# Optimization experiments

Measured on AMD Instinct MI355X. Metric: run time of the kernel, lower is better.

Reference implementation:

```python
import jax, jax.numpy as jnp
import numpy as np

D_MODEL = 1024
D_STATE = 16
D_CONV = 4
EXPAND = 2
HEADDIM = 8
D_INNER = EXPAND * D_MODEL            # 2048
NHEADS = D_INNER // HEADDIM           # 256
CONV_DIM = D_INNER + 2 * D_STATE      # 2080 (ngroups=1)
D_IN_PROJ = 2 * D_INNER + 2 * D_STATE + NHEADS  # 4384
B_SZ, SEQ = 4, 2048
EPS = 1e-5


def setup_inputs() -> dict:
    key = jax.random.key(0)
    ks = jax.random.split(key, 8)
    return {
        "x": jax.random.normal(ks[0], (B_SZ, SEQ, D_MODEL), jnp.float32),
        "ln_w": jnp.ones((D_MODEL,), jnp.float32),
        "ln_b": jnp.zeros((D_MODEL,), jnp.float32),
        "W_in": jax.random.normal(ks[1], (D_MODEL, D_IN_PROJ), jnp.float32) * 0.02,
        "conv_w": jax.random.normal(ks[2], (D_CONV, 1, CONV_DIM), jnp.float32) * 0.2,
        "conv_b": jnp.zeros((CONV_DIM,), jnp.float32),
        "A_log": jnp.log(jax.random.uniform(ks[3], (NHEADS,), jnp.float32, 1.0, 16.0)),
        "Dp": jnp.ones((NHEADS,), jnp.float32) + 0.1 * jax.random.normal(ks[4], (NHEADS,), jnp.float32),
        "dt_bias": 0.5 * jax.random.normal(ks[5], (NHEADS,), jnp.float32),
        "rms_w": jnp.ones((D_INNER,), jnp.float32),
        "W_out": jax.random.normal(ks[6], (D_INNER, D_MODEL), jnp.float32) * 0.02,
    }


def _mamba_block(x, ln_w, ln_b, W_in, conv_w, conv_b, A_log, Dp, dt_bias, rms_w, W_out):
    B, L, _ = x.shape
    # pre-norm LayerNorm
    mu = jnp.mean(x, axis=-1, keepdims=True)
    var = jnp.mean((x - mu) ** 2, axis=-1, keepdims=True)
    xn = (x - mu) * jax.lax.rsqrt(var + EPS) * ln_w + ln_b

    # in_proj -> z, xBC, dt
    u = xn @ W_in                                    # (B, L, 4384)
    z = u[..., :D_INNER]
    xBC = u[..., D_INNER:D_INNER + CONV_DIM]
    dt = jax.nn.softplus(u[..., -NHEADS:] + dt_bias)  # (B, L, NHEADS)

    # causal depthwise conv1d + SiLU
    xp = jnp.pad(xBC, ((0, 0), (D_CONV - 1, 0), (0, 0)))
    xBC = jax.lax.conv_general_dilated(
        xp, conv_w, window_strides=(1,), padding="VALID",
        dimension_numbers=("NWC", "WIO", "NWC"), feature_group_count=CONV_DIM)
    xBC = jax.nn.silu(xBC + conv_b)

    xs = xBC[..., :D_INNER].reshape(B, L, NHEADS, HEADDIM)   # SSM input
    Bm = xBC[..., D_INNER:D_INNER + D_STATE]                  # (B, L, N)
    Cm = xBC[..., D_INNER + D_STATE:]                          # (B, L, N)

    A = -jnp.exp(A_log)                                       # (NHEADS,)

    def step(h, inp):
        # h: (B, H, P, N)
        x_t, B_t, C_t, dt_t = inp
        dA = jnp.exp(dt_t * A)                                 # (B, H)
        h = h * dA[..., None, None] + jnp.einsum("bh,bhp,bn->bhpn", dt_t, x_t, B_t)
        y = jnp.einsum("bhpn,bn->bhp", h, C_t)
        return h, y

    h0 = jnp.zeros((B, NHEADS, HEADDIM, D_STATE), x.dtype)
    _, ys = jax.lax.scan(step, h0, (xs.swapaxes(0, 1), Bm.swapaxes(0, 1),
                                     Cm.swapaxes(0, 1), dt.swapaxes(0, 1)))
    y = ys.swapaxes(0, 1) + Dp[None, None, :, None] * xs       # (B, L, H, P)
    y = y.reshape(B, L, D_INNER)

    # gated RMSNorm: rmsnorm(y * silu(z)) * weight
    g = y * jax.nn.silu(z)
    g = g * jax.lax.rsqrt(jnp.mean(g * g, axis=-1, keepdims=True) + EPS) * rms_w

    return x + g @ W_out


def reference(x, ln_w, ln_b, W_in, conv_w, conv_b, A_log, Dp, dt_bias, rms_w, W_out):
    return _mamba_block(x, ln_w, ln_b, W_in, conv_w, conv_b, A_log, Dp, dt_bias, rms_w, W_out)
```

## Files before the change

kernel.cpp:

```cpp
#include <hip/hip_runtime.h>

typedef __bf16 bf16;
typedef __attribute__((ext_vector_type(8))) __bf16 bf16x8;
typedef __attribute__((ext_vector_type(4))) float f32x4;

#define B_SZ 4
#define SEQ 2048
#define DM 1024
#define DIN 2048
#define NH 256
#define DSTATE 16
#define CONVD 2080
#define DPROJ 4384
#define NPAD1 4608
#define MROWS 8192
#define NC 64
#define LC 32
#define UROWB 8768

__device__ __forceinline__ void gload_lds16(const void* g, void* l) {
  __builtin_amdgcn_global_load_lds(
      (__attribute__((address_space(1))) void*)g,
      (__attribute__((address_space(3))) void*)l, 16, 0, 0);
}

template <int N>
__device__ __forceinline__ void vm_wait() {
  asm volatile("s_waitcnt vmcnt(%0)" ::"n"(N) : "memory");
}
__device__ __forceinline__ void bar() { asm volatile("s_barrier" ::: "memory"); }
__device__ __forceinline__ void lgkm0() {
  asm volatile("s_waitcnt lgkmcnt(0)" ::: "memory");
}

__global__ void transpose_cvt(const float* __restrict__ W, bf16* __restrict__ WT,
                              int K, int N, int Npad) {
  __shared__ float tile[32][33];
  int k0 = blockIdx.x * 32, n0 = blockIdx.y * 32;
  int tx = threadIdx.x, ty = threadIdx.y;
#pragma unroll
  for (int j = 0; j < 4; j++) {
    int k = k0 + ty + 8 * j, n = n0 + tx;
    tile[ty + 8 * j][tx] = (k < K && n < N) ? W[(size_t)k * N + n] : 0.f;
  }
  __syncthreads();
#pragma unroll
  for (int j = 0; j < 4; j++) {
    int n = n0 + ty + 8 * j, k = k0 + tx;
    if (n < Npad && k < K) WT[(size_t)n * K + k] = (bf16)tile[tx][ty + 8 * j];
  }
}

__global__ __launch_bounds__(256) void ln_kernel(const float* __restrict__ x,
                                                 const float* __restrict__ lw,
                                                 const float* __restrict__ lb,
                                                 bf16* __restrict__ xn) {
  int row = blockIdx.x;
  int t = threadIdx.x;
  f32x4 v4 = ((const f32x4*)(x + (size_t)row * DM))[t];
  float v0 = v4[0], v1 = v4[1], v2 = v4[2], v3 = v4[3];
  float s = v0 + v1 + v2 + v3;
  float s2 = v0 * v0 + v1 * v1 + v2 * v2 + v3 * v3;
#pragma unroll
  for (int off = 32; off > 0; off >>= 1) {
    s += __shfl_down(s, off);
    s2 += __shfl_down(s2, off);
  }
  __shared__ float ps[8];
  int wave = t >> 6, lane = t & 63;
  if (lane == 0) { ps[wave] = s; ps[4 + wave] = s2; }
  __syncthreads();
  s = ps[0] + ps[1] + ps[2] + ps[3];
  s2 = ps[4] + ps[5] + ps[6] + ps[7];
  float mean = s * (1.f / DM);
  float var = s2 * (1.f / DM) - mean * mean;
  float rstd = rsqrtf(var + 1e-5f);
  f32x4 wv = ((const f32x4*)lw)[t];
  f32x4 bv = ((const f32x4*)lb)[t];
  bf16 o[4];
  o[0] = (bf16)((v0 - mean) * rstd * wv[0] + bv[0]);
  o[1] = (bf16)((v1 - mean) * rstd * wv[1] + bv[1]);
  o[2] = (bf16)((v2 - mean) * rstd * wv[2] + bv[2]);
  o[3] = (bf16)((v3 - mean) * rstd * wv[3] + bv[3]);
  bf16* dst = xn + (size_t)row * DM + t * 4;
  dst[0] = o[0]; dst[1] = o[1]; dst[2] = o[2]; dst[3] = o[3];
}

__global__ __launch_bounds__(512, 2) void gemm1_8p(const bf16* __restrict__ A,
                                                   const bf16* __restrict__ BT,
                                                   bf16* __restrict__ C) {
  __shared__ char lds[139264];
  int bid = blockIdx.x;
  int xcd = bid & 7;
  int l = bid >> 3;
  int bm = xcd * 4 + ((l >> 3) & 3);
  int bn = (l >> 5) * 8 + (l & 7);
  int m0 = bm * 256, n0 = bn * 192;
  int t = threadIdx.x, lane = t & 63, wave = t >> 6;
  int wm = wave >> 2, wn = wave & 3;
  int lr16 = lane & 15, kq = lane >> 4;
  int ts0 = kq ^ (lr16 & 7);
  int ts1 = (4 + kq) ^ (lr16 & 7);
  int sw = (lane & 7) ^ (lane >> 3);
  int l8 = lane >> 3;
  const char* Ab = (const char*)A;
  const char* Bb = (const char*)BT;

  auto stA = [&](int kt) {
    char* slot = lds + (kt & 1) * 32768;
    size_t ko = (size_t)kt * 128 + sw * 16;
#pragma unroll
    for (int g = 0; g < 4; g++) {
      int c = wave * 4 + g;
      gload_lds16(Ab + (size_t)(m0 + c * 8 + l8) * 2048 + ko, slot + c * 1024);
    }
  };
  auto stB = [&](int kt) {
    char* slot = lds + 65536 + (kt % 3) * 24576;
    size_t ko = (size_t)kt * 128 + sw * 16;
#pragma unroll
    for (int g = 0; g < 3; g++) {
      int c = wave * 3 + g;
      gload_lds16(Bb + (size_t)(n0 + c * 8 + l8) * 2048 + ko, slot + c * 1024);
    }
  };

  f32x4 acc[8][3] = {};
  bf16x8 a_[4][2], b_[3][2];

  stA(0); stB(0); stA(1); stB(1);
  vm_wait<7>();
  bar();
#pragma unroll 1
  for (int kt = 0; kt < 16; kt++) {
    {
      const char* sa = lds + (kt & 1) * 32768;
      const char* sb = lds + 65536 + (kt % 3) * 24576;
#pragma unroll
      for (int mi = 0; mi < 4; mi++) {
        int lrow = wm * 128 + mi * 16 + lr16;
        a_[mi][0] = *(const bf16x8*)(sa + lrow * 128 + ts0 * 16);
        a_[mi][1] = *(const bf16x8*)(sa + lrow * 128 + ts1 * 16);
      }
#pragma unroll
      for (int ni = 0; ni < 3; ni++) {
        int lrow = wn * 48 + ni * 16 + lr16;
        b_[ni][0] = *(const bf16x8*)(sb + lrow * 128 + ts0 * 16);
        b_[ni][1] = *(const bf16x8*)(sb + lrow * 128 + ts1 * 16);
      }
      if (kt >= 1 && kt < 15) stA(kt + 1);
      if (kt < 14) stB(kt + 2);
      bar();
      lgkm0();
      __builtin_amdgcn_s_setprio(1);
#pragma unroll
      for (int mi = 0; mi < 4; mi++)
#pragma unroll
        for (int ni = 0; ni < 3; ni++) {
          acc[mi][ni] = __builtin_amdgcn_mfma_f32_16x16x32_bf16(a_[mi][0], b_[ni][0], acc[mi][ni], 0, 0, 0);
          acc[mi][ni] = __builtin_amdgcn_mfma_f32_16x16x32_bf16(a_[mi][1], b_[ni][1], acc[mi][ni], 0, 0, 0);
        }
      __builtin_amdgcn_s_setprio(0);
      bar();
    }
    {
      const char* sa = lds + (kt & 1) * 32768;
#pragma unroll
      for (int mi = 0; mi < 4; mi++) {
        int lrow = wm * 128 + 64 + mi * 16 + lr16;
        a_[mi][0] = *(const bf16x8*)(sa + lrow * 128 + ts0 * 16);
        a_[mi][1] = *(const bf16x8*)(sa + lrow * 128 + ts1 * 16);
      }
      if (kt <= 13) vm_wait<3>();
      else if (kt == 14) vm_wait<0>();
      bar();
      lgkm0();
      __builtin_amdgcn_s_setprio(1);
#pragma unroll
      for (int mi = 0; mi < 4; mi++)
#pragma unroll
        for (int ni = 0; ni < 3; ni++) {
          acc[4 + mi][ni] = __builtin_amdgcn_mfma_f32_16x16x32_bf16(a_[mi][0], b_[ni][0], acc[4 + mi][ni], 0, 0, 0);
          acc[4 + mi][ni] = __builtin_amdgcn_mfma_f32_16x16x32_bf16(a_[mi][1], b_[ni][1], acc[4 + mi][ni], 0, 0, 0);
        }
      __builtin_amdgcn_s_setprio(0);
      bar();
    }
  }
#pragma unroll
  for (int fr = 0; fr < 8; fr++)
#pragma unroll
    for (int ni = 0; ni < 3; ni++) {
      int row = m0 + wm * 128 + fr * 16 + kq * 4;
      int col = n0 + wn * 48 + ni * 16 + lr16;
      f32x4 v = acc[fr][ni];
      if (col < 4384) {
#pragma unroll
        for (int r = 0; r < 4; r++)
          C[(size_t)(row + r) * DPROJ + col] = (bf16)v[r];
      }
    }
}

#define G2_PHASE(MQ, P, STAGE, VMW)                                                        \
  {                                                                                        \
    const char* sa_ = lds + ((P) * 2 + (MQ)) * 16384;                                      \
    const char* sb_ = lds + 65536 + (P) * 16384;                                           \
    bf16x8 a_[4][2], b_[2][2];                                                             \
    _Pragma("unroll") for (int mi = 0; mi < 4; mi++) {                                     \
      int lrow = wm * 64 + mi * 16 + lr16;                                                 \
      a_[mi][0] = *(const bf16x8*)(sa_ + lrow * 128 + ts0 * 16);                           \
      a_[mi][1] = *(const bf16x8*)(sa_ + lrow * 128 + ts1 * 16);                           \
    }                                                                                      \
    _Pragma("unroll") for (int ni = 0; ni < 2; ni++) {                                     \
      int lrow = wn * 32 + ni * 16 + lr16;                                                 \
      b_[ni][0] = *(const bf16x8*)(sb_ + lrow * 128 + ts0 * 16);                           \
      b_[ni][1] = *(const bf16x8*)(sb_ + lrow * 128 + ts1 * 16);                           \
    }                                                                                      \
    STAGE;                                                                                 \
    VMW;                                                                                   \
    bar();                                                                                 \
    lgkm0();                                                                               \
    __builtin_amdgcn_s_setprio(1);                                                         \
    _Pragma("unroll") for (int mi = 0; mi < 4; mi++)                                       \
      _Pragma("unroll") for (int ni = 0; ni < 2; ni++) {                                   \
        acc[(MQ) * 4 + mi][ni] = __builtin_amdgcn_mfma_f32_16x16x32_bf16(                  \
            a_[mi][0], b_[ni][0], acc[(MQ) * 4 + mi][ni], 0, 0, 0);                        \
        acc[(MQ) * 4 + mi][ni] = __builtin_amdgcn_mfma_f32_16x16x32_bf16(                  \
            a_[mi][1], b_[ni][1], acc[(MQ) * 4 + mi][ni], 0, 0, 0);                        \
      }                                                                                    \
    __builtin_amdgcn_s_setprio(0);                                                         \
    bar();                                                                                 \
  }

__global__ __launch_bounds__(512, 2) void gemm2_8p(const bf16* __restrict__ A,
                                                   const bf16* __restrict__ BT,
                                                   float* __restrict__ C,
                                                   const float* __restrict__ Xres) {
  __shared__ char lds[98304];
  int bid = blockIdx.x;
  int swz = (bid & 7) * 32 + (bid >> 3);
  int bm = swz >> 3, bn = swz & 7;
  int m0 = bm * 256, n0 = bn * 128;
  int t = threadIdx.x, lane = t & 63, wave = t >> 6;
  int wm = wave >> 2, wn = wave & 3;
  int lr16 = lane & 15, kq = lane >> 4;
  int ts0 = kq ^ (lr16 & 7);
  int ts1 = (4 + kq) ^ (lr16 & 7);
  int sw = (lane & 7) ^ ((lane >> 3) & 7);
  int l8 = lane >> 3;
  int c0 = 2 * wave, c1 = 2 * wave + 1;
  int lr0 = c0 * 8 + l8, lr1 = c1 * 8 + l8;
  const char* Ab = (const char*)A;
  const char* Bb = (const char*)BT;
  int grA0 = m0 + (lr0 >> 6) * 128 + (lr0 & 63);
  int grA1 = m0 + (lr1 >> 6) * 128 + (lr1 & 63);
  int gcB0 = n0 + lr0, gcB1 = n0 + lr1;

  auto stA = [&](int kt, int p, int mq) {
    char* slot = lds + (p * 2 + mq) * 16384;
    size_t ko = (size_t)kt * 128 + sw * 16;
    gload_lds16(Ab + (size_t)(grA0 + mq * 64) * 4096 + ko, slot + c0 * 1024);
    gload_lds16(Ab + (size_t)(grA1 + mq * 64) * 4096 + ko, slot + c1 * 1024);
  };
  auto stB = [&](int kt, int p) {
    char* slot = lds + 65536 + p * 16384;
    size_t ko = (size_t)kt * 128 + sw * 16;
    gload_lds16(Bb + (size_t)gcB0 * 4096 + ko, slot + c0 * 1024);
    gload_lds16(Bb + (size_t)gcB1 * 4096 + ko, slot + c1 * 1024);
  };

  f32x4 acc[8][2] = {};
  stA(0, 0, 0); stB(0, 0); stA(0, 0, 1); stA(1, 1, 0);
  vm_wait<4>();
  bar();
#pragma unroll 1
  for (int kt = 0; kt < 32; kt++) {
    int p = kt & 1;
    G2_PHASE(0, p, { if (kt + 1 < 32) { stB(kt + 1, p ^ 1); stA(kt + 1, p ^ 1, 1); } },
             { if (kt < 31) vm_wait<6>(); else vm_wait<0>(); });
    G2_PHASE(1, p, { if (kt + 2 < 32) stA(kt + 2, p, 0); },
             { if (kt < 30) vm_wait<4>(); else if (kt == 30) vm_wait<2>(); });
  }
#pragma unroll
  for (int mq = 0; mq < 2; mq++)
#pragma unroll
    for (int mi = 0; mi < 4; mi++)
#pragma unroll
      for (int ni = 0; ni < 2; ni++) {
        int row = m0 + wm * 128 + mq * 64 + mi * 16 + kq * 4;
        int col = n0 + wn * 32 + ni * 16 + lr16;
        f32x4 v = acc[mq * 4 + mi][ni];
#pragma unroll
        for (int r = 0; r < 4; r++) {
          size_t o = (size_t)(row + r) * DM + col;
          C[o] = Xres[o] + v[r];
        }
      }
}

__global__ __launch_bounds__(256) void conv_prep3(const bf16* __restrict__ u,
                                                  const float* __restrict__ cw,
                                                  const float* __restrict__ cb,
                                                  const float* __restrict__ dt_bias,
                                                  bf16* __restrict__ xs,
                                                  float* __restrict__ BC,
                                                  float* __restrict__ dtf) {
  const int JPR = 292;
  int idx = blockIdx.x * 256 + threadIdx.x;
  if (idx >= MROWS * JPR) return;
  int row = idx / JPR;
  int j = idx - row * JPR;
  int t = row & (SEQ - 1);
  if (j < 260) {
    int c0 = j * 8;
    float acc[8];
#pragma unroll
    for (int i = 0; i < 8; i++) acc[i] = cb[c0 + i];
    const bf16* ub = u + (size_t)row * DPROJ + DIN + c0;
#pragma unroll
    for (int tap = 0; tap < 4; tap++) {
      int tt = t - 3 + tap;
      if (tt >= 0) {
        bf16x8 uv = *(const bf16x8*)(ub + (ptrdiff_t)(tap - 3) * DPROJ);
        const float* wv = cw + tap * CONVD + c0;
#pragma unroll
        for (int i = 0; i < 8; i++) acc[i] += wv[i] * (float)uv[i];
      }
    }
    if (c0 < DIN) {
      bf16x8 o;
#pragma unroll
      for (int i = 0; i < 8; i++) {
        float sv = acc[i] / (1.f + __expf(-acc[i]));
        o[i] = (bf16)sv;
      }
      *(bf16x8*)(xs + (size_t)row * DIN + c0) = o;
    } else {
      float* bc = BC + (size_t)row * 32 + (c0 - DIN);
#pragma unroll
      for (int i = 0; i < 8; i++) bc[i] = acc[i] / (1.f + __expf(-acc[i]));
    }
  } else {
    int h0 = (j - 260) * 8;
    bf16x8 uv = *(const bf16x8*)(u + (size_t)row * DPROJ + (DPROJ - NH) + h0);
    float* dst = dtf + (size_t)row * NH + h0;
#pragma unroll
    for (int i = 0; i < 8; i++) {
      float xv = (float)uv[i] + dt_bias[h0 + i];
      dst[i] = (xv > 20.f) ? xv : log1pf(__expf(xv));
    }
  }
}

__global__ __launch_bounds__(64) void scan_p1(const bf16* __restrict__ xs,
                                              const float* __restrict__ BC,
                                              const float* __restrict__ dtf,
                                              const float* __restrict__ A_log,
                                              bf16* __restrict__ uscr) {
  int c = blockIdx.x & 63, hg = (blockIdx.x >> 6) & 31, b = blockIdx.x >> 11;
  int lane = threadIdx.x, hh = lane >> 3;
  int h = hg * 8 + hh;
  float A = -__expf(A_log[h]);
  float st[16];
#pragma unroll
  for (int n = 0; n < 16; n++) st[n] = 0.f;
  float pcum = 1.f;
  size_t rb = (size_t)b * SEQ + (size_t)c * LC;
  for (int t = 0; t < LC; t++) {
    size_t row = rb + t;
    const float* bcrow = BC + row * 32;
    float dtv = dtf[row * NH + h];
    float x = (float)xs[row * DIN + hg * 64 + lane];
    float dA = __expf(dtv * A);
    pcum *= dA;
    float w = dtv * x;
#pragma unroll
    for (int n = 0; n < 16; n++) st[n] = st[n] * dA + w * bcrow[n];
  }
  char* slot = (char*)uscr + (size_t)blockIdx.x * UROWB + 4096;
  float* S = (float*)slot;
#pragma unroll
  for (int n = 0; n < 16; n++) S[lane * 16 + n] = st[n];
  if ((lane & 7) == 0) ((float*)(slot + 4096))[hh] = pcum;
}

__global__ __launch_bounds__(64) void scan_p2(bf16* __restrict__ uscr) {
  int bh = blockIdx.x;
  int lane = threadIdx.x, hh = lane >> 3;
  float H[16];
#pragma unroll
  for (int n = 0; n < 16; n++) H[n] = 0.f;
  char* base = (char*)uscr + (size_t)bh * NC * UROWB + 4096;
  float sN[16], PN;
  {
    float* S = (float*)base;
#pragma unroll
    for (int n = 0; n < 16; n++) sN[n] = S[lane * 16 + n];
    PN = ((const float*)(base + 4096))[hh];
  }
  for (int c = 0; c < NC; c++) {
    float sC[16], PC = PN;
#pragma unroll
    for (int n = 0; n < 16; n++) sC[n] = sN[n];
    if (c + 1 < NC) {
      char* slot = base + (size_t)(c + 1) * UROWB;
      float* S = (float*)slot;
#pragma unroll
      for (int n = 0; n < 16; n++) sN[n] = S[lane * 16 + n];
      PN = ((const float*)(slot + 4096))[hh];
    }
    float* S0 = (float*)(base + (size_t)c * UROWB);
#pragma unroll
    for (int n = 0; n < 16; n++) {
      float hn = H[n];
      S0[lane * 16 + n] = hn;
      H[n] = PC * hn + sC[n];
    }
  }
}

__global__ __launch_bounds__(64) void scan_p3(const bf16* __restrict__ xs,
                                              const float* __restrict__ BC,
                                              const float* __restrict__ dtf,
                                              const float* __restrict__ A_log,
                                              const float* __restrict__ Dp,
                                              const bf16* __restrict__ uscr,
                                              bf16* __restrict__ y) {
  int c = blockIdx.x & 63, hg = (blockIdx.x >> 6) & 31, b = blockIdx.x >> 11;
  int lane = threadIdx.x, hh = lane >> 3;
  int h = hg * 8 + hh;
  float A = -__expf(A_log[h]);
  float D = Dp[h];
  const char* slot = (const char*)uscr + (size_t)blockIdx.x * UROWB + 4096;
  float st[16];
#pragma unroll
  for (int n = 0; n < 16; n++) st[n] = ((const float*)slot)[lane * 16 + n];
  size_t rb = (size_t)b * SEQ + (size_t)c * LC;
  for (int t = 0; t < LC; t++) {
    size_t row = rb + t;
    const float* bcrow = BC + row * 32;
    float dtv = dtf[row * NH + h];
    float x = (float)xs[row * DIN + hg * 64 + lane];
    float dA = __expf(dtv * A);
    float w = dtv * x;
    float yv = 0.f;
#pragma unroll
    for (int n = 0; n < 16; n++) {
      st[n] = st[n] * dA + w * bcrow[n];
      yv += st[n] * bcrow[16 + n];
    }
    y[row * DIN + hg * 64 + lane] = (bf16)(yv + D * x);
  }
}

__global__ __launch_bounds__(256) void gate_rms(const bf16* __restrict__ u,
                                                const bf16* __restrict__ y,
                                                const float* __restrict__ rms_w,
                                                bf16* __restrict__ g) {
  int row = blockIdx.x;
  int t = threadIdx.x;
  bf16x8 zv = ((const bf16x8*)(u + (size_t)row * DPROJ))[t];
  bf16x8 yv = ((const bf16x8*)(y + (size_t)row * DIN))[t];
  float gv[8];
  float s2 = 0.f;
#pragma unroll
  for (int i = 0; i < 8; i++) {
    float z = (float)zv[i];
    float yy = (float)yv[i];
    float gg = yy * z / (1.f + __expf(-z));
    gv[i] = gg;
    s2 += gg * gg;
  }
#pragma unroll
  for (int off = 32; off > 0; off >>= 1) s2 += __shfl_down(s2, off);
  __shared__ float ps[4];
  int wave = t >> 6, lane = t & 63;
  if (lane == 0) ps[wave] = s2;
  __syncthreads();
  s2 = ps[0] + ps[1] + ps[2] + ps[3];
  float scale = rsqrtf(s2 * (1.f / DIN) + 1e-5f);
  f32x4 w0 = ((const f32x4*)rms_w)[2 * t];
  f32x4 w1 = ((const f32x4*)rms_w)[2 * t + 1];
  bf16x8 og;
#pragma unroll
  for (int i = 0; i < 4; i++) og[i] = (bf16)(gv[i] * scale * w0[i]);
#pragma unroll
  for (int i = 0; i < 4; i++) og[4 + i] = (bf16)(gv[4 + i] * scale * w1[i]);
  ((bf16x8*)(g + (size_t)row * DIN))[t] = og;
}

extern "C" void kernel_launch(void* const* d_in, const int* in_sizes, int n_in,
                              void* d_out, int out_size, void* d_ws, size_t ws_size,
                              hipStream_t stream) {
  const float* x = (const float*)d_in[0];
  const float* lnw = (const float*)d_in[1];
  const float* lnb = (const float*)d_in[2];
  const float* Win = (const float*)d_in[3];
  const float* cw = (const float*)d_in[4];
  const float* cb = (const float*)d_in[5];
  const float* Alog = (const float*)d_in[6];
  const float* Dpv = (const float*)d_in[7];
  const float* dtb = (const float*)d_in[8];
  const float* rmsw = (const float*)d_in[9];
  const float* Wout = (const float*)d_in[10];
  float* out = (float*)d_out;

  char* ws = (char*)d_ws;
  bf16* u = (bf16*)(ws + 0);
  bf16* xnb = (bf16*)(ws + 71827456);
  bf16* WinT = (bf16*)(ws + 88604672);
  bf16* yb = (bf16*)(ws + 71827456);
  bf16* xsb = (bf16*)(ws + 105381888);
  bf16* gb = (bf16*)(ws + 105381888);
  float* BC = (float*)(ws + 138936320);
  float* dtf = (float*)(ws + 139984896);
  bf16* WoutT = (bf16*)(ws + 148373504);

  transpose_cvt<<<dim3(32, 144), dim3(32, 8), 0, stream>>>(Win, WinT, 1024, DPROJ, NPAD1);
  transpose_cvt<<<dim3(64, 32), dim3(32, 8), 0, stream>>>(Wout, WoutT, DIN, DM, DM);
  ln_kernel<<<MROWS, 256, 0, stream>>>(x, lnw, lnb, xnb);
  gemm1_8p<<<768, 512, 0, stream>>>(xnb, WinT, u);
  conv_prep3<<<(MROWS * 292) / 256, 256, 0, stream>>>(u, cw, cb, dtb, xsb, BC, dtf);
  scan_p1<<<MROWS, 64, 0, stream>>>(xsb, BC, dtf, Alog, u);
  scan_p2<<<128, 64, 0, stream>>>(u);
  scan_p3<<<MROWS, 64, 0, stream>>>(xsb, BC, dtf, Alog, Dpv, u, yb);
  gate_rms<<<MROWS, 256, 0, stream>>>(u, yb, rmsw, gb);
  gemm2_8p<<<256, 512, 0, stream>>>(gb, WoutT, out, x);
}
```

Before: 298.1 us.

## Retile out-projection GEMM to 128x256 with a three-stage LDS pipeline

Reshapes the out_proj GEMM block tile from 256x128 to 128x256. It replaces the two-buffer, split-phase staging scheme with a three-deep ring buffer, so loads are issued two k-steps ahead. Each k-step now computes in two halves over the B columns, with one combined prefetch per step. The goal is to hide global-to-LDS latency better and simplify the wait schedule. In exchange, LDS use rises to 144KB per block, which limits residency to one block per CU.

```diff
diff --git a/kernel.cpp b/kernel.cpp
--- a/kernel.cpp
+++ b/kernel.cpp
@@ -202,101 +202,117 @@
     }
 }
 
-#define G2_PHASE(MQ, P, STAGE, VMW)                                                        \
-  {                                                                                        \
-    const char* sa_ = lds + ((P) * 2 + (MQ)) * 16384;                                      \
-    const char* sb_ = lds + 65536 + (P) * 16384;                                           \
-    bf16x8 a_[4][2], b_[2][2];                                                             \
-    _Pragma("unroll") for (int mi = 0; mi < 4; mi++) {                                     \
-      int lrow = wm * 64 + mi * 16 + lr16;                                                 \
-      a_[mi][0] = *(const bf16x8*)(sa_ + lrow * 128 + ts0 * 16);                           \
-      a_[mi][1] = *(const bf16x8*)(sa_ + lrow * 128 + ts1 * 16);                           \
-    }                                                                                      \
-    _Pragma("unroll") for (int ni = 0; ni < 2; ni++) {                                     \
-      int lrow = wn * 32 + ni * 16 + lr16;                                                 \
-      b_[ni][0] = *(const bf16x8*)(sb_ + lrow * 128 + ts0 * 16);                           \
-      b_[ni][1] = *(const bf16x8*)(sb_ + lrow * 128 + ts1 * 16);                           \
-    }                                                                                      \
-    STAGE;                                                                                 \
-    VMW;                                                                                   \
-    bar();                                                                                 \
-    lgkm0();                                                                               \
-    __builtin_amdgcn_s_setprio(1);                                                         \
-    _Pragma("unroll") for (int mi = 0; mi < 4; mi++)                                       \
-      _Pragma("unroll") for (int ni = 0; ni < 2; ni++) {                                   \
-        acc[(MQ) * 4 + mi][ni] = __builtin_amdgcn_mfma_f32_16x16x32_bf16(                  \
-            a_[mi][0], b_[ni][0], acc[(MQ) * 4 + mi][ni], 0, 0, 0);                        \
-        acc[(MQ) * 4 + mi][ni] = __builtin_amdgcn_mfma_f32_16x16x32_bf16(                  \
-            a_[mi][1], b_[ni][1], acc[(MQ) * 4 + mi][ni], 0, 0, 0);                        \
-      }                                                                                    \
-    __builtin_amdgcn_s_setprio(0);                                                         \
-    bar();                                                                                 \
-  }
-
 __global__ __launch_bounds__(512, 2) void gemm2_8p(const bf16* __restrict__ A,
                                                    const bf16* __restrict__ BT,
                                                    float* __restrict__ C,
                                                    const float* __restrict__ Xres) {
-  __shared__ char lds[98304];
+  __shared__ char lds[147456];
   int bid = blockIdx.x;
   int swz = (bid & 7) * 32 + (bid >> 3);
-  int bm = swz >> 3, bn = swz & 7;
-  int m0 = bm * 256, n0 = bn * 128;
+  int bm = swz >> 2, bn = swz & 3;
+  int m0 = bm * 128, n0 = bn * 256;
   int t = threadIdx.x, lane = t & 63, wave = t >> 6;
   int wm = wave >> 2, wn = wave & 3;
   int lr16 = lane & 15, kq = lane >> 4;
   int ts0 = kq ^ (lr16 & 7);
   int ts1 = (4 + kq) ^ (lr16 & 7);
-  int sw = (lane & 7) ^ ((lane >> 3) & 7);
+  int sw = (lane & 7) ^ (lane >> 3);
   int l8 = lane >> 3;
-  int c0 = 2 * wave, c1 = 2 * wave + 1;
-  int lr0 = c0 * 8 + l8, lr1 = c1 * 8 + l8;
   const char* Ab = (const char*)A;
   const char* Bb = (const char*)BT;
-  int grA0 = m0 + (lr0 >> 6) * 128 + (lr0 & 63);
-  int grA1 = m0 + (lr1 >> 6) * 128 + (lr1 & 63);
-  int gcB0 = n0 + lr0, gcB1 = n0 + lr1;
-
-  auto stA = [&](int kt, int p, int mq) {
-    char* slot = lds + (p * 2 + mq) * 16384;
+
+  auto stA = [&](int kt) {
+    char* slot = lds + (kt % 3) * 16384;
     size_t ko = (size_t)kt * 128 + sw * 16;
-    gload_lds16(Ab + (size_t)(grA0 + mq * 64) * 4096 + ko, slot + c0 * 1024);
-    gload_lds16(Ab + (size_t)(grA1 + mq * 64) * 4096 + ko, slot + c1 * 1024);
+#pragma unroll
+    for (int g = 0; g < 2; g++) {
+      int c = wave * 2 + g;
+      gload_lds16(Ab + (size_t)(m0 + c * 8 + l8) * 4096 + ko, slot + c * 1024);
+    }
   };
-  auto stB = [&](int kt, int p) {
-    char* slot = lds + 65536 + p * 16384;
+  auto stB = [&](int kt) {
+    char* slot = lds + 49152 + (kt % 3) * 32768;
     size_t ko = (size_t)kt * 128 + sw * 16;
-    gload_lds16(Bb + (size_t)gcB0 * 4096 + ko, slot + c0 * 1024);
-    gload_lds16(Bb + (size_t)gcB1 * 4096 + ko, slot + c1 * 1024);
+#pragma unroll
+    for (int g = 0; g < 4; g++) {
+      int c = wave * 4 + g;
+      gload_lds16(Bb + (size_t)(n0 + c * 8 + l8) * 4096 + ko, slot + c * 1024);
+    }
   };
 
-  f32x4 acc[8][2] = {};
-  stA(0, 0, 0); stB(0, 0); stA(0, 0, 1); stA(1, 1, 0);
-  vm_wait<4>();
+  f32x4 acc[4][4] = {};
+  bf16x8 a_[4][2], b_[2][2];
+
+  stA(0); stB(0); stA(1); stB(1);
+  vm_wait<6>();
   bar();
 #pragma unroll 1
   for (int kt = 0; kt < 32; kt++) {
-    int p = kt & 1;
-    G2_PHASE(0, p, { if (kt + 1 < 32) { stB(kt + 1, p ^ 1); stA(kt + 1, p ^ 1, 1); } },
-             { if (kt < 31) vm_wait<6>(); else vm_wait<0>(); });
-    G2_PHASE(1, p, { if (kt + 2 < 32) stA(kt + 2, p, 0); },
-             { if (kt < 30) vm_wait<4>(); else if (kt == 30) vm_wait<2>(); });
-  }
-#pragma unroll
-  for (int mq = 0; mq < 2; mq++)
-#pragma unroll
-    for (int mi = 0; mi < 4; mi++)
+    const char* sa = lds + (kt % 3) * 16384;
+    const char* sb = lds + 49152 + (kt % 3) * 32768;
+    {
+#pragma unroll
+      for (int mi = 0; mi < 4; mi++) {
+        int lrow = wm * 64 + mi * 16 + lr16;
+        a_[mi][0] = *(const bf16x8*)(sa + lrow * 128 + ts0 * 16);
+        a_[mi][1] = *(const bf16x8*)(sa + lrow * 128 + ts1 * 16);
+      }
 #pragma unroll
       for (int ni = 0; ni < 2; ni++) {
-        int row = m0 + wm * 128 + mq * 64 + mi * 16 + kq * 4;
-        int col = n0 + wn * 32 + ni * 16 + lr16;
-        f32x4 v = acc[mq * 4 + mi][ni];
-#pragma unroll
-        for (int r = 0; r < 4; r++) {
-          size_t o = (size_t)(row + r) * DM + col;
-          C[o] = Xres[o] + v[r];
+        int lrow = wn * 64 + ni * 16 + lr16;
+        b_[ni][0] = *(const bf16x8*)(sb + lrow * 128 + ts0 * 16);
+        b_[ni][1] = *(const bf16x8*)(sb + lrow * 128 + ts1 * 16);
+      }
+      if (kt + 2 < 32) { stA(kt + 2); stB(kt + 2); }
+      bar();
+      lgkm0();
+      __builtin_amdgcn_s_setprio(1);
+#pragma unroll
+      for (int mi = 0; mi < 4; mi++)
+#pragma unroll
+        for (int ni = 0; ni < 2; ni++) {
+          acc[mi][ni] = __builtin_amdgcn_mfma_f32_16x16x32_bf16(a_[mi][0], b_[ni][0], acc[mi][ni], 0, 0, 0);
+          acc[mi][ni] = __builtin_amdgcn_mfma_f32_16x16x32_bf16(a_[mi][1], b_[ni][1], acc[mi][ni], 0, 0, 0);
         }
-      }
+      __builtin_amdgcn_s_setprio(0);
+      bar();
+    }
+    {
+#pragma unroll
+      for (int ni = 0; ni < 2; ni++) {
+        int lrow = wn * 64 + (2 + ni) * 16 + lr16;
+        b_[ni][0] = *(const bf16x8*)(sb + lrow * 128 + ts0 * 16);
+        b_[ni][1] = *(const bf16x8*)(sb + lrow * 128 + ts1 * 16);
+      }
+      if (kt <= 29) vm_wait<6>();
+      else if (kt == 30) vm_wait<0>();
+      bar();
+      lgkm0();
+      __builtin_amdgcn_s_setprio(1);
+#pragma unroll
+      for (int mi = 0; mi < 4; mi++)
+#pragma unroll
+        for (int ni = 0; ni < 2; ni++) {
+          acc[mi][2 + ni] = __builtin_amdgcn_mfma_f32_16x16x32_bf16(a_[mi][0], b_[ni][0], acc[mi][2 + ni], 0, 0, 0);
+          acc[mi][2 + ni] = __builtin_amdgcn_mfma_f32_16x16x32_bf16(a_[mi][1], b_[ni][1], acc[mi][2 + ni], 0, 0, 0);
+        }
+      __builtin_amdgcn_s_setprio(0);
+      bar();
+    }
+  }
+#pragma unroll
+  for (int mi = 0; mi < 4; mi++)
+#pragma unroll
+    for (int ni = 0; ni < 4; ni++) {
+      int row = m0 + wm * 64 + mi * 16 + kq * 4;
+      int col = n0 + wn * 64 + ni * 16 + lr16;
+      f32x4 v = acc[mi][ni];
+#pragma unroll
+      for (int r = 0; r < 4; r++) {
+        size_t o = (size_t)(row + r) * DM + col;
+        C[o] = Xres[o] + v[r];
+      }
+    }
 }
 
 __global__ __launch_bounds__(256) void conv_prep3(const bf16* __restrict__ u,
```

Result: no change. 296.8 us (-0.5%).
